# Kernel tuning notes

Hardware: AMD Instinct MI355X
Metric: run time of the kernel (lower is better)

## Reference

```python
import jax, jax.numpy as jnp
import numpy as np

HEADS = 16

def _binarize(W):
    # alpha: per-output-row mean of |W| (reduce over all dims except dim 0)
    alpha = jnp.mean(jnp.abs(W), axis=tuple(range(1, W.ndim)), keepdims=True)
    # straight-through sign: forward sign(W), backward identity
    B = W + jax.lax.stop_gradient(jnp.sign(W) - W)
    return alpha * B

def _binlinear(x, W, b):
    Wb = _binarize(W)
    return jnp.einsum('btc,oc->bto', x, Wb) + b

def setup_inputs() -> dict:
    key = jax.random.key(0)
    ks = jax.random.split(key, 9)
    dim = 1024
    B, T = 4, 2048
    inp = {
        'x': jax.random.normal(ks[0], (B, T, dim), jnp.float32),
        'Wq': jax.random.normal(ks[1], (dim, dim), jnp.float32) * 0.02,
        'bq': jax.random.normal(ks[2], (dim,), jnp.float32) * 0.02,
        'Wk': jax.random.normal(ks[3], (dim, dim), jnp.float32) * 0.02,
        'bk': jax.random.normal(ks[4], (dim,), jnp.float32) * 0.02,
        'Wv': jax.random.normal(ks[5], (dim, dim), jnp.float32) * 0.02,
        'bv': jax.random.normal(ks[6], (dim,), jnp.float32) * 0.02,
        'Wp': jax.random.normal(ks[7], (dim, dim), jnp.float32) * 0.02,
        'bp': jax.random.normal(ks[8], (dim,), jnp.float32) * 0.02,
    }
    return inp

def reference(x, Wq, bq, Wk, bk, Wv, bv, Wp, bp):
    B, T, C = x.shape
    H = HEADS
    Dh = C // H
    scale = Dh ** -0.5

    def split_heads(t):
        return t.reshape(B, T, H, Dh).transpose(0, 2, 1, 3)  # [B,H,T,Dh]

    q = split_heads(_binlinear(x, Wq, bq))
    k = split_heads(_binlinear(x, Wk, bk))
    v = split_heads(_binlinear(x, Wv, bv))

    att = jnp.einsum('bhtd,bhsd->bhts', q, k) * scale  # [B,H,T,T]
    att = jax.nn.softmax(att, axis=-1)
    y = jnp.einsum('bhts,bhsd->bhtd', att, v)  # [B,H,T,Dh]
    y = y.transpose(0, 2, 1, 3).reshape(B, T, C)
    return _binlinear(y, Wp, bp)
```

## Files before the change

### kernel.cpp

```cpp
#include <hip/hip_runtime.h>
#include <hip/hip_bf16.h>

typedef short s16x8 __attribute__((ext_vector_type(8)));
typedef float f32x4 __attribute__((ext_vector_type(4)));
typedef unsigned short u16;

#define LOG2E 1.4426950408889634f
#define QSC (0.125f * LOG2E)

typedef __attribute__((address_space(3))) unsigned int lds_u32;
typedef __attribute__((address_space(1))) const unsigned int glb_u32;

static __device__ __forceinline__ void gload16(const void* g, void* l) {
  __builtin_amdgcn_global_load_lds((glb_u32*)g, (lds_u32*)l, 16, 0, 0);
}
static __device__ __forceinline__ u16 bf16u(float f) {
  unsigned u = __builtin_bit_cast(unsigned, f);
  return (u16)((u + 0x7FFFu + ((u >> 16) & 1u)) >> 16);
}
static __device__ __forceinline__ unsigned pk(u16 a, u16 b) {
  return (unsigned)a | ((unsigned)b << 16);
}
static __device__ __forceinline__ unsigned pk2(float a, float b) {
  float2 f; f.x = a; f.y = b;
  __hip_bfloat162 h = __float22bfloat162_rn(f);
  unsigned r;
  __builtin_memcpy(&r, &h, 4);
  return r;
}

__global__ __launch_bounds__(256) void k_binarize(
    const float* __restrict__ Wq, const float* __restrict__ Wk,
    const float* __restrict__ Wv, const float* __restrict__ Wp,
    const float* __restrict__ bq, const float* __restrict__ bk,
    const float* __restrict__ bv, const float* __restrict__ bp,
    u16* __restrict__ wbqkv, u16* __restrict__ wbp,
    float* __restrict__ alphaf, float* __restrict__ biasf) {
  int wave = threadIdx.x >> 6, lane = threadIdx.x & 63;
  int row = blockIdx.x * 4 + wave;
  const float* src; const float* bias; int r;
  if (row < 1024)      { src = Wq; bias = bq; r = row; }
  else if (row < 2048) { src = Wk; bias = bk; r = row - 1024; }
  else if (row < 3072) { src = Wv; bias = bv; r = row - 2048; }
  else                 { src = Wp; bias = bp; r = row - 3072; }
  const float4* s4 = reinterpret_cast<const float4*>(src + r * 1024);
  float4 v[4];
  float asum = 0.f;
#pragma unroll
  for (int i = 0; i < 4; ++i) {
    v[i] = s4[lane * 4 + i];
    asum += fabsf(v[i].x) + fabsf(v[i].y) + fabsf(v[i].z) + fabsf(v[i].w);
  }
#pragma unroll
  for (int m = 32; m >= 1; m >>= 1) asum += __shfl_xor(asum, m, 64);
  float alpha = asum * (1.0f / 1024.0f);

  u16 o[16];
#pragma unroll
  for (int i = 0; i < 4; ++i) {
    const float* f = reinterpret_cast<const float*>(&v[i]);
#pragma unroll
    for (int j = 0; j < 4; ++j) {
      float w = f[j];
      o[i * 4 + j] = (w > 0.f) ? (u16)0x3F80 : ((w < 0.f) ? (u16)0xBF80 : (u16)0);
    }
  }
  u16* dst = (row < 3072 ? wbqkv + row * 1024 : wbp + (row - 3072) * 1024) + lane * 16;
  uint4 w0 = { pk(o[0],o[1]), pk(o[2],o[3]), pk(o[4],o[5]), pk(o[6],o[7]) };
  uint4 w1 = { pk(o[8],o[9]), pk(o[10],o[11]), pk(o[12],o[13]), pk(o[14],o[15]) };
  reinterpret_cast<uint4*>(dst)[0] = w0;
  reinterpret_cast<uint4*>(dst)[1] = w1;
  if (lane == 0) {
    float sc = (row < 1024) ? QSC : 1.0f;
    alphaf[row] = alpha * sc;
    biasf[row]  = bias[r] * sc;
  }
}

__global__ __launch_bounds__(256) void k_cvt(const float* __restrict__ x, u16* __restrict__ xb) {
  int i = (blockIdx.x * 256 + threadIdx.x) * 8;
  float4 a = *reinterpret_cast<const float4*>(x + i);
  float4 b = *reinterpret_cast<const float4*>(x + i + 4);
  uint4 w = { pk(bf16u(a.x), bf16u(a.y)), pk(bf16u(a.z), bf16u(a.w)),
              pk(bf16u(b.x), bf16u(b.y)), pk(bf16u(b.z), bf16u(b.w)) };
  *reinterpret_cast<uint4*>(xb + i) = w;
}

template <int MODE>
__global__ __launch_bounds__(256) void k_gemm(
    const u16* __restrict__ A, const u16* __restrict__ Bw,
    const float* __restrict__ alphaf, const float* __restrict__ biasf,
    u16* __restrict__ qbuf, u16* __restrict__ kbuf, u16* __restrict__ vtbuf,
    float* __restrict__ outf) {
  __shared__ alignas(128) char smem[33792];
  char* As = smem;
  char* Bs = smem + 16384;
  int tid = threadIdx.x;
  int wave = tid >> 6, l = tid & 63, g = l >> 4, ln = l & 15;
  int wm = (wave >> 1) * 64, wn = (wave & 1) * 64;
  int m0 = blockIdx.y * 128, n0 = blockIdx.x * 128;

  f32x4 acc[4][4];
#pragma unroll
  for (int i = 0; i < 4; ++i)
#pragma unroll
    for (int j = 0; j < 4; ++j) acc[i][j] = f32x4{0.f, 0.f, 0.f, 0.f};

  const char* Ab = reinterpret_cast<const char*>(A) + m0 * 2048;
  const char* Bb = reinterpret_cast<const char*>(Bw) + n0 * 2048;

  int soff[4];
#pragma unroll
  for (int i = 0; i < 4; ++i) {
    int P = i * 4096 + tid * 16;
    int r = P >> 7;
    int kc = ((P >> 4) & 7) ^ (r & 7);
    soff[i] = r * 2048 + kc * 16;
  }

  for (int ks = 0; ks < 16; ++ks) {
    int kb0 = ks * 128;
#pragma unroll
    for (int i = 0; i < 4; ++i)
      gload16(Ab + soff[i] + kb0, As + i * 4096 + wave * 1024);
#pragma unroll
    for (int i = 0; i < 4; ++i)
      gload16(Bb + soff[i] + kb0, Bs + i * 4096 + wave * 1024);
    __syncthreads();
#pragma unroll
    for (int kk = 0; kk < 2; ++kk) {
      s16x8 af[4], bfr[4];
#pragma unroll
      for (int mf = 0; mf < 4; ++mf) {
        int r = wm + mf * 16 + ln;
        int kb = (kk * 64 + g * 16) ^ ((r & 7) << 4);
        af[mf] = *reinterpret_cast<const s16x8*>(As + r * 128 + kb);
      }
#pragma unroll
      for (int nf = 0; nf < 4; ++nf) {
        int r = wn + nf * 16 + ln;
        int kb = (kk * 64 + g * 16) ^ ((r & 7) << 4);
        bfr[nf] = *reinterpret_cast<const s16x8*>(Bs + r * 128 + kb);
      }
#pragma unroll
      for (int mf = 0; mf < 4; ++mf)
#pragma unroll
        for (int nf = 0; nf < 4; ++nf)
          acc[mf][nf] = __builtin_amdgcn_mfma_f32_16x16x32_bf16(af[mf], bfr[nf], acc[mf][nf], 0, 0, 0);
    }
    __syncthreads();
  }

  if (MODE == 0) {
    if (n0 < 2048) {
      u16* dst = (n0 < 1024) ? qbuf : kbuf;
#pragma unroll
      for (int nf = 0; nf < 4; ++nf) {
        int n = n0 + wn + nf * 16 + ln;
        float al = alphaf[n], bi = biasf[n];
        int nl = n & 1023;
        int h = nl >> 6, d = nl & 63;
#pragma unroll
        for (int mf = 0; mf < 4; ++mf)
#pragma unroll
          for (int rg = 0; rg < 4; ++rg) {
            int m = m0 + wm + mf * 16 + g * 4 + rg;
            int b = m >> 11, t = m & 2047;
            dst[(((b * 16 + h) * 2048 + t) << 6) + d] = bf16u(al * acc[mf][nf][rg] + bi);
          }
      }
    } else {
      u16* ldsT = reinterpret_cast<u16*>(smem);
#pragma unroll
      for (int nf = 0; nf < 4; ++nf) {
        int n = n0 + wn + nf * 16 + ln;
        float al = alphaf[n], bi = biasf[n];
        int nloc = wn + nf * 16 + ln;
#pragma unroll
        for (int mf = 0; mf < 4; ++mf)
#pragma unroll
          for (int rg = 0; rg < 4; ++rg) {
            int mloc = wm + mf * 16 + g * 4 + rg;
            ldsT[mloc * 132 + nloc] = bf16u(al * acc[mf][nf][rg] + bi);
          }
      }
      __syncthreads();
      int dl = tid >> 1;
      int sh = (tid & 1) * 64;
      int nv = n0 - 2048 + dl;
      int h = nv >> 6, d = nv & 63;
      int b = m0 >> 11;
      int s0 = (m0 & 2047) + sh;
      u16* vdst = vtbuf + (((b * 16 + h) * 64 + d) << 11) + s0;
#pragma unroll
      for (int c8 = 0; c8 < 8; ++c8) {
        u16 t0 = ldsT[(sh + c8 * 8 + 0) * 132 + dl], t1 = ldsT[(sh + c8 * 8 + 1) * 132 + dl];
        u16 t2 = ldsT[(sh + c8 * 8 + 2) * 132 + dl], t3 = ldsT[(sh + c8 * 8 + 3) * 132 + dl];
        u16 t4 = ldsT[(sh + c8 * 8 + 4) * 132 + dl], t5 = ldsT[(sh + c8 * 8 + 5) * 132 + dl];
        u16 t6 = ldsT[(sh + c8 * 8 + 6) * 132 + dl], t7 = ldsT[(sh + c8 * 8 + 7) * 132 + dl];
        uint4 w = { pk(t0, t1), pk(t2, t3), pk(t4, t5), pk(t6, t7) };
        *reinterpret_cast<uint4*>(vdst + c8 * 8) = w;
      }
    }
  } else {
#pragma unroll
    for (int nf = 0; nf < 4; ++nf) {
      int n = n0 + wn + nf * 16 + ln;
      float al = alphaf[3072 + n], bi = biasf[3072 + n];
#pragma unroll
      for (int mf = 0; mf < 4; ++mf)
#pragma unroll
        for (int rg = 0; rg < 4; ++rg) {
          int m = m0 + wm + mf * 16 + g * 4 + rg;
          outf[m * 1024 + n] = al * acc[mf][nf][rg] + bi;
        }
    }
  }
}

__global__ __launch_bounds__(512, 4) void k_attn(
    const u16* __restrict__ qb, const u16* __restrict__ kb,
    const u16* __restrict__ vtb, u16* __restrict__ yb) {
  __shared__ alignas(128) char smem[65536];
  int tid = threadIdx.x;
  int wave = tid >> 6, lane = tid & 63;
  int g = lane >> 4, ln = lane & 15;
  int swz = (ln & 7) << 4;

  int wg = (blockIdx.x & 7) * 64 + (blockIdx.x >> 3);
  int bh = wg >> 3, qt = wg & 7;
  const char* Qg = reinterpret_cast<const char*>(qb) + bh * 262144;
  const char* Kg = reinterpret_cast<const char*>(kb) + bh * 262144;
  const char* Vg = reinterpret_cast<const char*>(vtb) + bh * 262144;

  int qrow = qt * 256 + wave * 32 + ln;
  const s16x8* Qr0 = reinterpret_cast<const s16x8*>(Qg + qrow * 128);
  const s16x8* Qr1 = reinterpret_cast<const s16x8*>(Qg + (qrow + 16) * 128);
  s16x8 qf[2][2];
  qf[0][0] = Qr0[g]; qf[0][1] = Qr0[g + 4];
  qf[1][0] = Qr1[g]; qf[1][1] = Qr1[g + 4];

  s16x8 ones;
#pragma unroll
  for (int i = 0; i < 8; ++i) ones[i] = (short)0x3F80;

  int r = tid >> 3, kc = tid & 7;
  int swsrc = (kc ^ (r & 7)) * 16;
  int ksrc = r * 128 + swsrc;
  int vsrc = r * 4096 + swsrc;

  char* Ps = smem + 32768 + wave * 4096;

  f32x4 oacc[2][4];
#pragma unroll
  for (int s = 0; s < 2; ++s)
#pragma unroll
    for (int i = 0; i < 4; ++i) oacc[s][i] = f32x4{0.f, 0.f, 0.f, 0.f};
  f32x4 lacc[2];
  lacc[0] = f32x4{0.f, 0.f, 0.f, 0.f};
  lacc[1] = f32x4{0.f, 0.f, 0.f, 0.f};

  gload16(Kg + ksrc, smem + wave * 1024);
  gload16(Vg + vsrc, smem + 8192 + wave * 1024);
  __syncthreads();

  for (int st = 0; st < 32; ++st) {
    int cb = st & 1;
    if (st < 31) {
      int sb = (st + 1) * 64;
      char* nb = smem + (cb ^ 1) * 16384;
      gload16(Kg + sb * 128 + ksrc, nb + wave * 1024);
      gload16(Vg + sb * 2 + vsrc, nb + 8192 + wave * 1024);
    }
    const char* Kb = smem + cb * 16384;
    const char* Vb = Kb + 8192;

    f32x4 sacc[2][4];
#pragma unroll
    for (int s = 0; s < 2; ++s)
#pragma unroll
      for (int t = 0; t < 4; ++t) sacc[s][t] = f32x4{0.f, 0.f, 0.f, 0.f};
    __builtin_amdgcn_s_setprio(1);
#pragma unroll
    for (int kt = 0; kt < 2; ++kt) {
      int off = (kt * 64 + g * 16) ^ swz;
#pragma unroll
      for (int t = 0; t < 4; ++t) {
        s16x8 kf = *reinterpret_cast<const s16x8*>(Kb + (t * 16 + ln) * 128 + off);
        sacc[0][t] = __builtin_amdgcn_mfma_f32_16x16x32_bf16(kf, qf[0][kt], sacc[0][t], 0, 0, 0);
        sacc[1][t] = __builtin_amdgcn_mfma_f32_16x16x32_bf16(kf, qf[1][kt], sacc[1][t], 0, 0, 0);
      }
    }
    __builtin_amdgcn_s_setprio(0);

#pragma unroll
    for (int s = 0; s < 2; ++s) {
      char* Pr = Ps + (s * 16 + ln) * 128;
#pragma unroll
      for (int t = 0; t < 4; ++t) {
        float e0 = __builtin_amdgcn_exp2f(sacc[s][t][0]);
        float e1 = __builtin_amdgcn_exp2f(sacc[s][t][1]);
        float e2 = __builtin_amdgcn_exp2f(sacc[s][t][2]);
        float e3 = __builtin_amdgcn_exp2f(sacc[s][t][3]);
        uint2 w;
        w.x = pk2(e0, e1);
        w.y = pk2(e2, e3);
        *reinterpret_cast<uint2*>(Pr + ((t * 32 + g * 8) ^ swz)) = w;
      }
    }

    s16x8 pf[2][2];
#pragma unroll
    for (int s = 0; s < 2; ++s) {
      const char* Pr = Ps + (s * 16 + ln) * 128;
      pf[s][0] = *reinterpret_cast<const s16x8*>(Pr + ((g * 16) ^ swz));
      pf[s][1] = *reinterpret_cast<const s16x8*>(Pr + ((64 + g * 16) ^ swz));
    }

#pragma unroll
    for (int s = 0; s < 2; ++s)
#pragma unroll
      for (int kt = 0; kt < 2; ++kt)
        lacc[s] = __builtin_amdgcn_mfma_f32_16x16x32_bf16(ones, pf[s][kt], lacc[s], 0, 0, 0);

    __builtin_amdgcn_s_setprio(1);
#pragma unroll
    for (int kt = 0; kt < 2; ++kt) {
      int off = (kt * 64 + g * 16) ^ swz;
#pragma unroll
      for (int dt = 0; dt < 4; ++dt) {
        s16x8 vf = *reinterpret_cast<const s16x8*>(Vb + (dt * 16 + ln) * 128 + off);
        oacc[0][dt] = __builtin_amdgcn_mfma_f32_16x16x32_bf16(vf, pf[0][kt], oacc[0][dt], 0, 0, 0);
        oacc[1][dt] = __builtin_amdgcn_mfma_f32_16x16x32_bf16(vf, pf[1][kt], oacc[1][dt], 0, 0, 0);
      }
    }
    __builtin_amdgcn_s_setprio(0);
    __syncthreads();
  }

  int b = bh >> 4, h = bh & 15;
#pragma unroll
  for (int s = 0; s < 2; ++s) {
    float linv = 1.0f / lacc[s][0];
    u16* yrow = yb + (b * 2048 + qrow + s * 16) * 1024 + h * 64;
#pragma unroll
    for (int dt = 0; dt < 4; ++dt) {
      uint2 w;
      w.x = pk2(oacc[s][dt][0] * linv, oacc[s][dt][1] * linv);
      w.y = pk2(oacc[s][dt][2] * linv, oacc[s][dt][3] * linv);
      *reinterpret_cast<uint2*>(yrow + dt * 16 + g * 4) = w;
    }
  }
}

extern "C" void kernel_launch(void* const* d_in, const int* in_sizes, int n_in,
                              void* d_out, int out_size, void* d_ws, size_t ws_size,
                              hipStream_t stream) {
  (void)in_sizes; (void)n_in; (void)out_size; (void)ws_size;
  const float* x  = (const float*)d_in[0];
  const float* Wq = (const float*)d_in[1];
  const float* bq = (const float*)d_in[2];
  const float* Wk = (const float*)d_in[3];
  const float* bk = (const float*)d_in[4];
  const float* Wv = (const float*)d_in[5];
  const float* bv = (const float*)d_in[6];
  const float* Wp = (const float*)d_in[7];
  const float* bp = (const float*)d_in[8];

  char* ws = (char*)d_ws;
  u16*   xb    = (u16*)(ws);
  u16*   wbqkv = (u16*)(ws + 16777216);
  u16*   wbp   = (u16*)(ws + 23068672);
  float* alphaf = (float*)(ws + 25165824);
  float* biasf  = (float*)(ws + 25182208);
  u16*   vtbuf = (u16*)(ws + 25198592);
  u16*   ybuf  = xb;
  u16*   qbuf  = (u16*)d_out;
  u16*   kbuf  = (u16*)d_out + 8388608;
  float* outf  = (float*)d_out;

  k_binarize<<<1024, 256, 0, stream>>>(Wq, Wk, Wv, Wp, bq, bk, bv, bp, wbqkv, wbp, alphaf, biasf);
  k_cvt<<<4096, 256, 0, stream>>>(x, xb);
  k_gemm<0><<<dim3(24, 64), 256, 0, stream>>>(xb, wbqkv, alphaf, biasf, qbuf, kbuf, vtbuf, nullptr);
  k_attn<<<512, 512, 0, stream>>>(qbuf, kbuf, vtbuf, ybuf);
  k_gemm<1><<<dim3(8, 64), 256, 0, stream>>>(ybuf, wbp, alphaf, biasf, nullptr, nullptr, nullptr, outf);
}
```

Before: 181.0 us.

## Fuse prep kernels, remap GEMM workgroups across XCDs, prefetch V fragments

Merges the weight binarize and x-to-bf16 conversion into one launch, which removes a kernel launch and its gap. Both GEMMs switch to a 1D grid whose block index is remapped so that consecutive tiles land on the same XCD (blockIdx mod 8), aiming for better L2 reuse of A and B tiles. In attention, the V fragments are loaded from LDS into registers before the softmax and P stores, so the LDS latency overlaps the exp work. The cost is higher register pressure in the attention loop.

```diff
diff --git a/kernel.cpp b/kernel.cpp
--- a/kernel.cpp
+++ b/kernel.cpp
@@ -29,13 +29,22 @@
   return r;
 }
 
-__global__ __launch_bounds__(256) void k_binarize(
+__global__ __launch_bounds__(256) void k_prep(
+    const float* __restrict__ x, u16* __restrict__ xb,
     const float* __restrict__ Wq, const float* __restrict__ Wk,
     const float* __restrict__ Wv, const float* __restrict__ Wp,
     const float* __restrict__ bq, const float* __restrict__ bk,
     const float* __restrict__ bv, const float* __restrict__ bp,
     u16* __restrict__ wbqkv, u16* __restrict__ wbp,
     float* __restrict__ alphaf, float* __restrict__ biasf) {
+  if (blockIdx.x >= 1024) {
+    int i = ((blockIdx.x - 1024) * 256 + threadIdx.x) * 8;
+    float4 a = *reinterpret_cast<const float4*>(x + i);
+    float4 b = *reinterpret_cast<const float4*>(x + i + 4);
+    uint4 w = { pk2(a.x, a.y), pk2(a.z, a.w), pk2(b.x, b.y), pk2(b.z, b.w) };
+    *reinterpret_cast<uint4*>(xb + i) = w;
+    return;
+  }
   int wave = threadIdx.x >> 6, lane = threadIdx.x & 63;
   int row = blockIdx.x * 4 + wave;
   const float* src; const float* bias; int r;
@@ -77,16 +86,7 @@
   }
 }
 
-__global__ __launch_bounds__(256) void k_cvt(const float* __restrict__ x, u16* __restrict__ xb) {
-  int i = (blockIdx.x * 256 + threadIdx.x) * 8;
-  float4 a = *reinterpret_cast<const float4*>(x + i);
-  float4 b = *reinterpret_cast<const float4*>(x + i + 4);
-  uint4 w = { pk(bf16u(a.x), bf16u(a.y)), pk(bf16u(a.z), bf16u(a.w)),
-              pk(bf16u(b.x), bf16u(b.y)), pk(bf16u(b.z), bf16u(b.w)) };
-  *reinterpret_cast<uint4*>(xb + i) = w;
-}
-
-template <int MODE>
+template <int MODE, int NX, int NWG>
 __global__ __launch_bounds__(256) void k_gemm(
     const u16* __restrict__ A, const u16* __restrict__ Bw,
     const float* __restrict__ alphaf, const float* __restrict__ biasf,
@@ -98,7 +98,8 @@
   int tid = threadIdx.x;
   int wave = tid >> 6, l = tid & 63, g = l >> 4, ln = l & 15;
   int wm = (wave >> 1) * 64, wn = (wave & 1) * 64;
-  int m0 = blockIdx.y * 128, n0 = blockIdx.x * 128;
+  int wg = (blockIdx.x & 7) * (NWG / 8) + (blockIdx.x >> 3);
+  int m0 = (wg / NX) * 128, n0 = (wg % NX) * 128;
 
   f32x4 acc[4][4];
 #pragma unroll
@@ -292,6 +293,15 @@
       }
     }
     __builtin_amdgcn_s_setprio(0);
+
+    s16x8 vfr[2][4];
+#pragma unroll
+    for (int kt = 0; kt < 2; ++kt) {
+      int off = (kt * 64 + g * 16) ^ swz;
+#pragma unroll
+      for (int dt = 0; dt < 4; ++dt)
+        vfr[kt][dt] = *reinterpret_cast<const s16x8*>(Vb + (dt * 16 + ln) * 128 + off);
+    }
 
 #pragma unroll
     for (int s = 0; s < 2; ++s) {
@@ -326,12 +336,10 @@
     __builtin_amdgcn_s_setprio(1);
 #pragma unroll
     for (int kt = 0; kt < 2; ++kt) {
-      int off = (kt * 64 + g * 16) ^ swz;
 #pragma unroll
       for (int dt = 0; dt < 4; ++dt) {
-        s16x8 vf = *reinterpret_cast<const s16x8*>(Vb + (dt * 16 + ln) * 128 + off);
-        oacc[0][dt] = __builtin_amdgcn_mfma_f32_16x16x32_bf16(vf, pf[0][kt], oacc[0][dt], 0, 0, 0);
-        oacc[1][dt] = __builtin_amdgcn_mfma_f32_16x16x32_bf16(vf, pf[1][kt], oacc[1][dt], 0, 0, 0);
+        oacc[0][dt] = __builtin_amdgcn_mfma_f32_16x16x32_bf16(vfr[kt][dt], pf[0][kt], oacc[0][dt], 0, 0, 0);
+        oacc[1][dt] = __builtin_amdgcn_mfma_f32_16x16x32_bf16(vfr[kt][dt], pf[1][kt], oacc[1][dt], 0, 0, 0);
       }
     }
     __builtin_amdgcn_s_setprio(0);
@@ -379,9 +387,8 @@
   u16*   kbuf  = (u16*)d_out + 8388608;
   float* outf  = (float*)d_out;
 
-  k_binarize<<<1024, 256, 0, stream>>>(Wq, Wk, Wv, Wp, bq, bk, bv, bp, wbqkv, wbp, alphaf, biasf);
-  k_cvt<<<4096, 256, 0, stream>>>(x, xb);
-  k_gemm<0><<<dim3(24, 64), 256, 0, stream>>>(xb, wbqkv, alphaf, biasf, qbuf, kbuf, vtbuf, nullptr);
+  k_prep<<<5120, 256, 0, stream>>>(x, xb, Wq, Wk, Wv, Wp, bq, bk, bv, bp, wbqkv, wbp, alphaf, biasf);
+  k_gemm<0, 24, 1536><<<1536, 256, 0, stream>>>(xb, wbqkv, alphaf, biasf, qbuf, kbuf, vtbuf, nullptr);
   k_attn<<<512, 512, 0, stream>>>(qbuf, kbuf, vtbuf, ybuf);
-  k_gemm<1><<<dim3(8, 64), 256, 0, stream>>>(ybuf, wbp, alphaf, biasf, nullptr, nullptr, nullptr, outf);
-}
+  k_gemm<1, 8, 512><<<512, 256, 0, stream>>>(ybuf, wbp, alphaf, biasf, nullptr, nullptr, nullptr, outf);
+}
```

Measured after the change: 174.5 us. 1.04x faster.
